# Kernel optimization log

Hardware: AMD Instinct MI355X
Metric: run time of the kernel (lower is better)

## Reference

```python
import jax, jax.numpy as jnp
import numpy as np

N_NODES = 10000
N_EDGES = 160000
N_HEADS = 2
N_IN = 16   # fc input dim = x channels (15) + 1 dist channel
N_OUT = 32
ALPHA = 0.2
B, T_LEN = 2, 8


def setup_inputs() -> dict:
    key = jax.random.key(0)
    ks = jax.random.split(key, 6)
    x = jax.random.normal(ks[0], (B, T_LEN, N_NODES, N_IN - 1), dtype=jnp.float32)
    d_ew = jax.random.uniform(ks[1], (N_EDGES + N_NODES, N_HEADS), dtype=jnp.float32)
    u_edges = jax.random.randint(ks[2], (N_EDGES, 2), 0, N_NODES, dtype=jnp.int64)
    u_dist = jax.random.uniform(ks[3], (N_EDGES,), dtype=jnp.float32)
    W = jax.random.normal(ks[4], (N_OUT, N_IN), dtype=jnp.float32) * (1.0 / np.sqrt(N_IN))
    b = jax.random.normal(ks[5], (N_OUT,), dtype=jnp.float32) * 0.01
    return {"x": x, "T": T_LEN, "d_ew": d_ew, "u_edges": u_edges,
            "u_dist": u_dist, "W": W, "b": b}


def reference(x, T, d_ew, u_edges, u_dist, W, b):
    # d_edges = [u_edges; self-loops], d_dist = [u_dist; zeros]
    loops = jnp.arange(N_NODES, dtype=u_edges.dtype)
    d_edges = jnp.concatenate([u_edges, jnp.stack([loops, loops], axis=1)], axis=0)
    d_dist = jnp.concatenate([u_dist, jnp.zeros((N_NODES,), dtype=u_dist.dtype)], axis=0)
    node_i, node_j = d_edges[:, 0], d_edges[:, 1]

    Bx, t, _, C = x.shape
    # graph convolution: out[:, :, j] = sum_e{j(e)=j} d_ew[e] * x[:, :, i(e)]
    xg = x[:, :, node_i, :]                               # (B, t, E, C)
    msgs = xg[..., None, :] * d_ew[None, None, :, :, None]  # (B, t, E, H, C)
    x_conv = jnp.zeros((Bx, t, N_NODES, N_HEADS, C), dtype=x.dtype)
    x_conv = x_conv.at[:, :, node_j].add(msgs)            # (B, t, N, H, C)

    # dist convolution: (N, H)
    dist_conv = jnp.zeros((N_NODES, N_HEADS), dtype=d_ew.dtype)
    dist_conv = dist_conv.at[node_j].add(d_dist[:, None] * d_ew)

    # concat dist channel, broadcast over (B, t)
    dist_b = jnp.broadcast_to(dist_conv[None, None, :, :, None],
                              (Bx, t, N_NODES, N_HEADS, 1))
    x_feature = jnp.concatenate([x_conv, dist_b], axis=-1)  # (B, t, N, H, C+1)

    x_out = jnp.einsum('btnhc,oc->btnho', x_feature, W) + b

    # temporal alpha-blend (RHS uses pre-update values, as in torch slice assign)
    x_out = jnp.concatenate(
        [x_out[:, :1], ALPHA * x_out[:, :-1] + (1.0 - ALPHA) * x_out[:, 1:]], axis=1)
    return jax.nn.sigmoid(x_out)
```

## Files before the change

### kernel.cpp

```cpp
#include <hip/hip_runtime.h>
#include <hip/hip_bf16.h>

#define NN 10000
#define NE 160000
#define NBT 16
#define CIN 15
#define HPAD 128
#define BCAP 64
#define NOUT 32
#define ALPHA_F 0.2f

#define TRANS_BLKS 625
#define EDGE_BLKS  625

__device__ __forceinline__ float bf2f(unsigned short u) {
    return __uint_as_float(((unsigned int)u) << 16);
}
__device__ __forceinline__ unsigned short f2bf(float f) {
    __hip_bfloat16 h = __float2bfloat16(f);
    return *(unsigned short*)&h;
}

__global__ __launch_bounds__(256) void zero_ws(int* __restrict__ p) {
    int i = blockIdx.x * 256 + threadIdx.x;
    if (i < NN) p[i] = 0;
}

__global__ __launch_bounds__(256) void prep(const float* __restrict__ x,
                                            const int* __restrict__ edges,
                                            const float* __restrict__ dist,
                                            const float* __restrict__ dew,
                                            unsigned short* __restrict__ xh,
                                            int* __restrict__ cursor,
                                            int2* __restrict__ epay) {
    __shared__ float tile[NBT][16 * CIN];
    int bid = blockIdx.x;
    int tid = threadIdx.x;
    if (bid < TRANS_BLKS) {
        int n0 = bid * 16;
        if (tid < 16 * CIN) {
#pragma unroll
            for (int bt = 0; bt < NBT; ++bt)
                tile[bt][tid] = x[((size_t)bt * NN + n0) * CIN + tid];
        }
        __syncthreads();
        for (int g = tid; g < 16 * 256; g += 256) {
            int ln = g >> 8;
            int r  = g & 255;
            int c  = r & 15;
            int bt = r >> 4;
            float v = (c < 15) ? tile[bt][ln * CIN + c] : 0.f;
            xh[(size_t)(n0 + ln) * 256 + r] = f2bf(v);
        }
    } else {
        int e = (bid - TRANS_BLKS) * 256 + tid;
        if (e < NE) {
            int2 ed = ((const int2*)edges)[e];
            float2 w = ((const float2*)dew)[e];
            float d = dist[e];
            int pos = atomicAdd(&cursor[ed.y], 1);
            if (pos < BCAP) {
                unsigned int px = (unsigned int)ed.x | ((unsigned int)f2bf(d) << 16);
                unsigned int py = (unsigned int)f2bf(w.x) | ((unsigned int)f2bf(w.y) << 16);
                epay[ed.y * BCAP + pos] = make_int2((int)px, (int)py);
            }
        }
    }
}

__global__ __launch_bounds__(256) void fused_node(const unsigned short* __restrict__ xh,
                                                  const int* __restrict__ cursor,
                                                  const int2* __restrict__ epay,
                                                  const float* __restrict__ dew,
                                                  const float* __restrict__ W,
                                                  const float* __restrict__ bias,
                                                  float* __restrict__ out) {
    __shared__ float s_xc[4][2][256];

    const int tid = threadIdx.x;
    const int unit = tid >> 6;
    const int lane = tid & 63;
    const int n = blockIdx.x * 4 + unit;
    const int o = lane & 31;
    const int h = lane >> 5;
    const bool ispad = (lane & 3) == 3;

    float4 w0_ = *(const float4*)(W + o * 16);
    float4 w1_ = *(const float4*)(W + o * 16 + 4);
    float4 w2_ = *(const float4*)(W + o * 16 + 8);
    float4 w3_ = *(const float4*)(W + o * 16 + 12);
    float bo = bias[o];

    int deg = cursor[n];
    if (deg > BCAP) deg = BCAP;

    int2 pay = epay[n * BCAP + (lane & 31)];

    const char* xbase = (const char*)xh + 8 * lane;
    float a00 = 0.f, a01 = 0.f, a02 = 0.f, a03 = 0.f;
    float a10 = 0.f, a11 = 0.f, a12 = 0.f, a13 = 0.f;

    int dmain = deg > 32 ? 32 : deg;
#pragma unroll 8
    for (int k = 0; k < dmain; ++k) {
        int sx = __builtin_amdgcn_readlane(pay.x, k);
        int sw = __builtin_amdgcn_readlane(pay.y, k);
        uint2 u = *(const uint2*)(xbase + (size_t)((sx & 0xFFFF) << 9));
        float w0 = __uint_as_float((unsigned int)sw << 16);
        float w1 = __uint_as_float((unsigned int)sw & 0xFFFF0000u);
        float de = __uint_as_float((unsigned int)sx & 0xFFFF0000u);
        float x0 = __uint_as_float(u.x << 16);
        float x1 = __uint_as_float(u.x & 0xFFFF0000u);
        float x2 = __uint_as_float(u.y << 16);
        float x3 = ispad ? de : __uint_as_float(u.y & 0xFFFF0000u);
        a00 += w0 * x0; a01 += w0 * x1; a02 += w0 * x2; a03 += w0 * x3;
        a10 += w1 * x0; a11 += w1 * x1; a12 += w1 * x2; a13 += w1 * x3;
    }
    if (deg > 32) {
        int2 pay2 = epay[n * BCAP + 32 + (lane & 31)];
        for (int k = 32; k < deg; ++k) {
            int sx = __builtin_amdgcn_readlane(pay2.x, k - 32);
            int sw = __builtin_amdgcn_readlane(pay2.y, k - 32);
            uint2 u = *(const uint2*)(xbase + (size_t)((sx & 0xFFFF) << 9));
            float w0 = __uint_as_float((unsigned int)sw << 16);
            float w1 = __uint_as_float((unsigned int)sw & 0xFFFF0000u);
            float de = __uint_as_float((unsigned int)sx & 0xFFFF0000u);
            float x0 = __uint_as_float(u.x << 16);
            float x1 = __uint_as_float(u.x & 0xFFFF0000u);
            float x2 = __uint_as_float(u.y << 16);
            float x3 = ispad ? de : __uint_as_float(u.y & 0xFFFF0000u);
            a00 += w0 * x0; a01 += w0 * x1; a02 += w0 * x2; a03 += w0 * x3;
            a10 += w1 * x0; a11 += w1 * x1; a12 += w1 * x2; a13 += w1 * x3;
        }
    }
    {
        uint2 u = *(const uint2*)(xbase + ((size_t)n << 9));
        float w0 = dew[2 * (NE + n) + 0];
        float w1 = dew[2 * (NE + n) + 1];
        float x0 = __uint_as_float(u.x << 16);
        float x1 = __uint_as_float(u.x & 0xFFFF0000u);
        float x2 = __uint_as_float(u.y << 16);
        float x3 = __uint_as_float(u.y & 0xFFFF0000u);
        a00 += w0 * x0; a01 += w0 * x1; a02 += w0 * x2; a03 += w0 * x3;
        a10 += w1 * x0; a11 += w1 * x1; a12 += w1 * x2; a13 += w1 * x3;
    }
    *(float4*)&s_xc[unit][0][4 * lane] = make_float4(a00, a01, a02, a03);
    *(float4*)&s_xc[unit][1][4 * lane] = make_float4(a10, a11, a12, a13);

    asm volatile("s_waitcnt lgkmcnt(0)" ::: "memory");

    {
        float Wr[16] = { w0_.x, w0_.y, w0_.z, w0_.w,
                         w1_.x, w1_.y, w1_.z, w1_.w,
                         w2_.x, w2_.y, w2_.z, w2_.w,
                         w3_.x, w3_.y, w3_.z, w3_.w };
        const float* xc = s_xc[unit][h];
#pragma unroll
        for (int b = 0; b < 2; ++b) {
            float prev = 0.f;
#pragma unroll
            for (int t = 0; t < 8; ++t) {
                const float* xt = xc + b * HPAD + t * 16;
                float4 v0 = *(const float4*)(xt);
                float4 v1 = *(const float4*)(xt + 4);
                float4 v2 = *(const float4*)(xt + 8);
                float4 v3 = *(const float4*)(xt + 12);
                float y = bo;
                y += Wr[0]*v0.x + Wr[1]*v0.y + Wr[2]*v0.z + Wr[3]*v0.w;
                y += Wr[4]*v1.x + Wr[5]*v1.y + Wr[6]*v1.z + Wr[7]*v1.w;
                y += Wr[8]*v2.x + Wr[9]*v2.y + Wr[10]*v2.z + Wr[11]*v2.w;
                y += Wr[12]*v3.x + Wr[13]*v3.y + Wr[14]*v3.z + Wr[15]*v3.w;
                float v = (t == 0) ? y : (ALPHA_F * prev + (1.f - ALPHA_F) * y);
                float sg = 1.f / (1.f + __expf(-v));
                __builtin_nontemporal_store(sg,
                    &out[(((size_t)(b * 8 + t) * NN + n) * 2 + h) * NOUT + o]);
                prev = y;
            }
        }
    }
}

extern "C" void kernel_launch(void* const* d_in, const int* in_sizes, int n_in,
                              void* d_out, int out_size, void* d_ws, size_t ws_size,
                              hipStream_t stream) {
    const float* x     = (const float*)d_in[0];
    const float* dew   = (const float*)d_in[2];
    const int*   edges = (const int*)d_in[3];
    const float* dist  = (const float*)d_in[4];
    const float* W     = (const float*)d_in[5];
    const float* bias  = (const float*)d_in[6];
    float* out = (float*)d_out;

    unsigned short* xh = (unsigned short*)d_ws;
    int2* epay   = (int2*)(xh + (size_t)NN * 256);
    int* cursor  = (int*)(epay + (size_t)NN * BCAP);

    zero_ws<<<(NN + 255) / 256, 256, 0, stream>>>(cursor);
    prep<<<TRANS_BLKS + EDGE_BLKS, 256, 0, stream>>>(x, edges, dist, dew,
                                                     xh, cursor, epay);
    fused_node<<<2500, 256, 0, stream>>>(xh, cursor, epay, dew, W, bias, out);
}
```

Measured before the change: 50.44 us.

## Split node kernel across batch halves to double block count

Each node's work in the fused kernel is now split across two blocks, one per batch index. Each lane gathers 4 bytes (2 channels) instead of 8, and the grid doubles to 5000 blocks. Paired blocks sit next to each other in block order so they share gathered rows in cache. The aim is more parallelism and latency hiding for the gather. In exchange, each block repeats the edge payload readlanes and weight loads, doubling that overhead.

Measured after the change: 53.27 us. 5.6% more time.

```diff
diff --git a/kernel.cpp b/kernel.cpp
--- a/kernel.cpp
+++ b/kernel.cpp
@@ -75,15 +75,18 @@
                                                   const float* __restrict__ W,
                                                   const float* __restrict__ bias,
                                                   float* __restrict__ out) {
-    __shared__ float s_xc[4][2][256];
+    __shared__ float s_xc[4][2][HPAD];
 
     const int tid = threadIdx.x;
     const int unit = tid >> 6;
     const int lane = tid & 63;
-    const int n = blockIdx.x * 4 + unit;
+    const int bid = blockIdx.x;
+    const int hf = (bid & 7) >> 2;
+    const int gidHalf = (bid >> 3) * 4 + (bid & 3);
+    const int n = gidHalf * 4 + unit;
     const int o = lane & 31;
     const int h = lane >> 5;
-    const bool ispad = (lane & 3) == 3;
+    const bool ispad = (lane & 7) == 7;
 
     float4 w0_ = *(const float4*)(W + o * 16);
     float4 w1_ = *(const float4*)(W + o * 16 + 4);
@@ -96,56 +99,49 @@
 
     int2 pay = epay[n * BCAP + (lane & 31)];
 
-    const char* xbase = (const char*)xh + 8 * lane;
-    float a00 = 0.f, a01 = 0.f, a02 = 0.f, a03 = 0.f;
-    float a10 = 0.f, a11 = 0.f, a12 = 0.f, a13 = 0.f;
+    const char* xbase = (const char*)xh + hf * 256 + 4 * lane;
+    float a00 = 0.f, a01 = 0.f, a10 = 0.f, a11 = 0.f;
 
     int dmain = deg > 32 ? 32 : deg;
 #pragma unroll 8
     for (int k = 0; k < dmain; ++k) {
         int sx = __builtin_amdgcn_readlane(pay.x, k);
         int sw = __builtin_amdgcn_readlane(pay.y, k);
-        uint2 u = *(const uint2*)(xbase + (size_t)((sx & 0xFFFF) << 9));
+        unsigned int u = *(const unsigned int*)(xbase + (size_t)((sx & 0xFFFF) << 9));
         float w0 = __uint_as_float((unsigned int)sw << 16);
         float w1 = __uint_as_float((unsigned int)sw & 0xFFFF0000u);
         float de = __uint_as_float((unsigned int)sx & 0xFFFF0000u);
-        float x0 = __uint_as_float(u.x << 16);
-        float x1 = __uint_as_float(u.x & 0xFFFF0000u);
-        float x2 = __uint_as_float(u.y << 16);
-        float x3 = ispad ? de : __uint_as_float(u.y & 0xFFFF0000u);
-        a00 += w0 * x0; a01 += w0 * x1; a02 += w0 * x2; a03 += w0 * x3;
-        a10 += w1 * x0; a11 += w1 * x1; a12 += w1 * x2; a13 += w1 * x3;
+        float x0 = __uint_as_float(u << 16);
+        float x1 = ispad ? de : __uint_as_float(u & 0xFFFF0000u);
+        a00 += w0 * x0; a01 += w0 * x1;
+        a10 += w1 * x0; a11 += w1 * x1;
     }
     if (deg > 32) {
         int2 pay2 = epay[n * BCAP + 32 + (lane & 31)];
         for (int k = 32; k < deg; ++k) {
             int sx = __builtin_amdgcn_readlane(pay2.x, k - 32);
             int sw = __builtin_amdgcn_readlane(pay2.y, k - 32);
-            uint2 u = *(const uint2*)(xbase + (size_t)((sx & 0xFFFF) << 9));
+            unsigned int u = *(const unsigned int*)(xbase + (size_t)((sx & 0xFFFF) << 9));
             float w0 = __uint_as_float((unsigned int)sw << 16);
             float w1 = __uint_as_float((unsigned int)sw & 0xFFFF0000u);
             float de = __uint_as_float((unsigned int)sx & 0xFFFF0000u);
-            float x0 = __uint_as_float(u.x << 16);
-            float x1 = __uint_as_float(u.x & 0xFFFF0000u);
-            float x2 = __uint_as_float(u.y << 16);
-            float x3 = ispad ? de : __uint_as_float(u.y & 0xFFFF0000u);
-            a00 += w0 * x0; a01 += w0 * x1; a02 += w0 * x2; a03 += w0 * x3;
-            a10 += w1 * x0; a11 += w1 * x1; a12 += w1 * x2; a13 += w1 * x3;
+            float x0 = __uint_as_float(u << 16);
+            float x1 = ispad ? de : __uint_as_float(u & 0xFFFF0000u);
+            a00 += w0 * x0; a01 += w0 * x1;
+            a10 += w1 * x0; a11 += w1 * x1;
         }
     }
     {
-        uint2 u = *(const uint2*)(xbase + ((size_t)n << 9));
+        unsigned int u = *(const unsigned int*)(xbase + ((size_t)n << 9));
         float w0 = dew[2 * (NE + n) + 0];
         float w1 = dew[2 * (NE + n) + 1];
-        float x0 = __uint_as_float(u.x << 16);
-        float x1 = __uint_as_float(u.x & 0xFFFF0000u);
-        float x2 = __uint_as_float(u.y << 16);
-        float x3 = __uint_as_float(u.y & 0xFFFF0000u);
-        a00 += w0 * x0; a01 += w0 * x1; a02 += w0 * x2; a03 += w0 * x3;
-        a10 += w1 * x0; a11 += w1 * x1; a12 += w1 * x2; a13 += w1 * x3;
+        float x0 = __uint_as_float(u << 16);
+        float x1 = __uint_as_float(u & 0xFFFF0000u);
+        a00 += w0 * x0; a01 += w0 * x1;
+        a10 += w1 * x0; a11 += w1 * x1;
     }
-    *(float4*)&s_xc[unit][0][4 * lane] = make_float4(a00, a01, a02, a03);
-    *(float4*)&s_xc[unit][1][4 * lane] = make_float4(a10, a11, a12, a13);
+    *(float2*)&s_xc[unit][0][2 * lane] = make_float2(a00, a01);
+    *(float2*)&s_xc[unit][1][2 * lane] = make_float2(a10, a11);
 
     asm volatile("s_waitcnt lgkmcnt(0)" ::: "memory");
 
@@ -155,27 +151,24 @@
                          w2_.x, w2_.y, w2_.z, w2_.w,
                          w3_.x, w3_.y, w3_.z, w3_.w };
         const float* xc = s_xc[unit][h];
+        float prev = 0.f;
 #pragma unroll
-        for (int b = 0; b < 2; ++b) {
-            float prev = 0.f;
-#pragma unroll
-            for (int t = 0; t < 8; ++t) {
-                const float* xt = xc + b * HPAD + t * 16;
-                float4 v0 = *(const float4*)(xt);
-                float4 v1 = *(const float4*)(xt + 4);
-                float4 v2 = *(const float4*)(xt + 8);
-                float4 v3 = *(const float4*)(xt + 12);
-                float y = bo;
-                y += Wr[0]*v0.x + Wr[1]*v0.y + Wr[2]*v0.z + Wr[3]*v0.w;
-                y += Wr[4]*v1.x + Wr[5]*v1.y + Wr[6]*v1.z + Wr[7]*v1.w;
-                y += Wr[8]*v2.x + Wr[9]*v2.y + Wr[10]*v2.z + Wr[11]*v2.w;
-                y += Wr[12]*v3.x + Wr[13]*v3.y + Wr[14]*v3.z + Wr[15]*v3.w;
-                float v = (t == 0) ? y : (ALPHA_F * prev + (1.f - ALPHA_F) * y);
-                float sg = 1.f / (1.f + __expf(-v));
-                __builtin_nontemporal_store(sg,
-                    &out[(((size_t)(b * 8 + t) * NN + n) * 2 + h) * NOUT + o]);
-                prev = y;
-            }
+        for (int t = 0; t < 8; ++t) {
+            const float* xt = xc + t * 16;
+            float4 v0 = *(const float4*)(xt);
+            float4 v1 = *(const float4*)(xt + 4);
+            float4 v2 = *(const float4*)(xt + 8);
+            float4 v3 = *(const float4*)(xt + 12);
+            float y = bo;
+            y += Wr[0]*v0.x + Wr[1]*v0.y + Wr[2]*v0.z + Wr[3]*v0.w;
+            y += Wr[4]*v1.x + Wr[5]*v1.y + Wr[6]*v1.z + Wr[7]*v1.w;
+            y += Wr[8]*v2.x + Wr[9]*v2.y + Wr[10]*v2.z + Wr[11]*v2.w;
+            y += Wr[12]*v3.x + Wr[13]*v3.y + Wr[14]*v3.z + Wr[15]*v3.w;
+            float v = (t == 0) ? y : (ALPHA_F * prev + (1.f - ALPHA_F) * y);
+            float sg = 1.f / (1.f + __expf(-v));
+            __builtin_nontemporal_store(sg,
+                &out[(((size_t)(hf * 8 + t) * NN + n) * 2 + h) * NOUT + o]);
+            prev = y;
         }
     }
 }
@@ -198,5 +191,5 @@
     zero_ws<<<(NN + 255) / 256, 256, 0, stream>>>(cursor);
     prep<<<TRANS_BLKS + EDGE_BLKS, 256, 0, stream>>>(x, edges, dist, dew,
                                                      xh, cursor, epay);
-    fused_node<<<2500, 256, 0, stream>>>(xh, cursor, epay, dew, W, bias, out);
+    fused_node<<<5000, 256, 0, stream>>>(xh, cursor, epay, dew, W, bias, out);
 }
```
